# Performance work log

Measured on AMD Instinct MI355X. Metric: run time of the kernel, lower is better.

Reference implementation:

```python
import jax, jax.numpy as jnp
import numpy as np

H = 8          # n_heads
SIZE = 512     # model size
HEAD = SIZE // H
EPS = 1e-5

def _layer_norm(x, g, b):
    mu = jnp.mean(x, axis=-1, keepdims=True)
    var = jnp.var(x, axis=-1, keepdims=True)
    return (x - mu) * jax.lax.rsqrt(var + EPS) * g + b

def setup_inputs() -> dict:
    key = jax.random.key(0)
    ks = jax.random.split(key, 7)
    B, Lq, Lkv, Dq, Dkv = 16, 1024, 1024, 512, 512
    w = 0.02
    return {
        "query": jax.random.normal(ks[0], (B, Lq, Dq), jnp.float32),
        "key_value": jax.random.normal(ks[1], (B, Lkv, Dkv), jnp.float32),
        "Wq": jax.random.normal(ks[2], (SIZE, Dq), jnp.float32) * w,
        "bq": jnp.zeros((SIZE,), jnp.float32),
        "Wk": jax.random.normal(ks[3], (SIZE, Dkv), jnp.float32) * w,
        "bk": jnp.zeros((SIZE,), jnp.float32),
        "Wv": jax.random.normal(ks[4], (SIZE, Dkv), jnp.float32) * w,
        "bv": jnp.zeros((SIZE,), jnp.float32),
        "Wo": jax.random.normal(ks[5], (SIZE, SIZE), jnp.float32) * w,
        "bo": jnp.zeros((SIZE,), jnp.float32),
        "g0": jnp.ones((SIZE,), jnp.float32),
        "b0": jnp.zeros((SIZE,), jnp.float32),
        "g1": jnp.ones((SIZE,), jnp.float32),
        "b1": jnp.zeros((SIZE,), jnp.float32),
    }

def reference(query, key_value, Wq, bq, Wk, bk, Wv, bv, Wo, bo, g0, b0, g1, b1):
    B, Lq, _ = query.shape
    Lkv = key_value.shape[1]
    q = query @ Wq.T + bq            # [B, Lq, SIZE]
    k = key_value @ Wk.T + bk        # [B, Lkv, SIZE]
    v = key_value @ Wv.T + bv        # [B, Lkv, SIZE]
    # split heads along feature dim (equivalent to torch cat(split, 0))
    qh = q.reshape(B, Lq, H, HEAD)
    kh = k.reshape(B, Lkv, H, HEAD)
    vh = v.reshape(B, Lkv, H, HEAD)
    # NOTE: original scales by sqrt(size), NOT sqrt(head_size)
    scores = jnp.einsum('bqhd,bkhd->bhqk', qh, kh) / jnp.sqrt(jnp.float32(SIZE))
    A = jax.nn.softmax(scores, axis=-1)              # [B, H, Lq, Lkv]
    attn = jnp.einsum('bhqk,bkhd->bqhd', A, vh)      # [B, Lq, H, HEAD]
    out = (qh + attn).reshape(B, Lq, SIZE)           # residual uses projected q
    out = _layer_norm(out, g0, b0)
    out = out + jax.nn.relu(out @ Wo.T + bo)
    out = _layer_norm(out, g1, b1)
    return out
```

## Files before the change

### kernel.cpp

```cpp
#include <hip/hip_runtime.h>
#include <hip/hip_bf16.h>


#define HNUM 8
#define MSIZE 512
#define HEADD 64
#define LQ 1024
#define LKV 1024
#define NBATCH 16

typedef unsigned short u16;
typedef __bf16 bf16_t;
typedef bf16_t bf16x8 __attribute__((ext_vector_type(8)));
typedef float f32x4 __attribute__((ext_vector_type(4)));
typedef u16 u16x8 __attribute__((ext_vector_type(8)));

__device__ __forceinline__ u16 f2bf(float f) {
  __bf16 h = (__bf16)f;
  u16 r; __builtin_memcpy(&r, &h, 2); return r;
}

__device__ __forceinline__ bf16x8 ldb8(const void* p) {
  bf16x8 r; __builtin_memcpy(&r, p, 16); return r;
}
__device__ __forceinline__ float4 ldf4(const float* p) {
  float4 v; __builtin_memcpy(&v, p, 16); return v;
}
__device__ __forceinline__ void stf4(float* p, const float4& v) {
  __builtin_memcpy(p, &v, 16);
}

__device__ __forceinline__ void gload16(const u16* g, u16* l) {
  __builtin_amdgcn_global_load_lds((const __attribute__((address_space(1))) void*)g,
                                   (__attribute__((address_space(3))) void*)l,
                                   16, 0, 0);
}


__global__ __launch_bounds__(256) void cvt2_k(const float* __restrict__ a, u16* __restrict__ da,
                                              const float* __restrict__ b, u16* __restrict__ db,
                                              int n) {
  size_t i = ((size_t)blockIdx.x * 256 + threadIdx.x) * 8;
  const float* s; u16* d;
  if (i < (size_t)n) { s = a + i; d = da + i; }
  else               { s = b + (i - n); d = db + (i - n); }
  float4 v0 = ldf4(s), v1 = ldf4(s + 4);
  u16x8 o;
  o[0]=f2bf(v0.x); o[1]=f2bf(v0.y); o[2]=f2bf(v0.z); o[3]=f2bf(v0.w);
  o[4]=f2bf(v1.x); o[5]=f2bf(v1.y); o[6]=f2bf(v1.z); o[7]=f2bf(v1.w);
  __builtin_memcpy(d, &o, 16);
}

__global__ __launch_bounds__(256) void cvt4_k(const float* __restrict__ a0, u16* __restrict__ d0,
                                              const float* __restrict__ a1, u16* __restrict__ d1,
                                              const float* __restrict__ a2, u16* __restrict__ d2,
                                              const float* __restrict__ a3, u16* __restrict__ d3,
                                              int n) {
  size_t i = ((size_t)blockIdx.x * 256 + threadIdx.x) * 8;
  int sel = (int)(i / (size_t)n);
  size_t off = i - (size_t)sel * (size_t)n;
  const float* s = sel == 0 ? a0 : sel == 1 ? a1 : sel == 2 ? a2 : a3;
  u16*         d = sel == 0 ? d0 : sel == 1 ? d1 : sel == 2 ? d2 : d3;
  float4 v0 = ldf4(s + off), v1 = ldf4(s + off + 4);
  u16x8 o;
  o[0]=f2bf(v0.x); o[1]=f2bf(v0.y); o[2]=f2bf(v0.z); o[3]=f2bf(v0.w);
  o[4]=f2bf(v1.x); o[5]=f2bf(v1.y); o[6]=f2bf(v1.z); o[7]=f2bf(v1.w);
  __builtin_memcpy(d + off, &o, 16);
}


template<int MODE>
__global__ __launch_bounds__(256) void gemm_bt_k(
    const u16* __restrict__ A, const u16* __restrict__ W, const float* __restrict__ bias,
    const float* __restrict__ resid, float* __restrict__ outf, u16* __restrict__ outb)
{
  __shared__ u16 As[128 * 32];
  __shared__ u16 Bs[128 * 32];
  const int tid = threadIdx.x;
  const int w = tid >> 6, l = tid & 63;
  const int wr = w >> 1, wc = w & 1;
  const int lo = l & 15, hi = l >> 4;
  const int mb = blockIdx.y, nb = blockIdx.x;

  f32x4 acc[4][4] = {};
  const int s0 = w * 128 + l;

  for (int kt = 0; kt < 16; ++kt) {
    __syncthreads();
#pragma unroll
    for (int c = 0; c < 2; ++c) {
      int s = s0 + c * 64;
      int row = s >> 2, k8 = s & 3;
      const u16* ga = A + (size_t)(mb * 128 + row) * MSIZE + kt * 32 + k8 * 8;
      gload16(ga, &As[(w * 128 + c * 64) * 8]);
      const u16* gw = W + (size_t)(nb * 128 + row) * MSIZE + kt * 32 + k8 * 8;
      gload16(gw, &Bs[(w * 128 + c * 64) * 8]);
    }
    __syncthreads();
    bf16x8 af[4], bfr[4];
#pragma unroll
    for (int i = 0; i < 4; ++i) af[i]  = ldb8(&As[(wr * 64 + i * 16 + lo) * 32 + hi * 8]);
#pragma unroll
    for (int j = 0; j < 4; ++j) bfr[j] = ldb8(&Bs[(wc * 64 + j * 16 + lo) * 32 + hi * 8]);
#pragma unroll
    for (int i = 0; i < 4; ++i)
#pragma unroll
      for (int j = 0; j < 4; ++j)
        acc[i][j] = __builtin_amdgcn_mfma_f32_16x16x32_bf16(af[i], bfr[j], acc[i][j], 0, 0, 0);
  }

  const int nbase = nb * 128 + wc * 64;
  const int mbase = mb * 128 + wr * 64;
  float bj[4];
#pragma unroll
  for (int j = 0; j < 4; ++j) bj[j] = bias[nbase + j * 16 + lo];

  if (MODE == 2) {
    u16* T = As;
#pragma unroll
    for (int j = 0; j < 4; ++j) {
      __syncthreads();
#pragma unroll
      for (int i = 0; i < 4; ++i)
#pragma unroll
        for (int e = 0; e < 4; ++e) {
          int n_local = wc * 16 + lo;
          int m_local = wr * 64 + i * 16 + hi * 4 + e;
          T[n_local * 128 + m_local] = f2bf(acc[i][j][e] + bj[j]);
        }
      __syncthreads();
      int n_local = tid >> 3, m0 = (tid & 7) * 16;
      u16x8 r0, r1;
      __builtin_memcpy(&r0, &T[n_local * 128 + m0], 16);
      __builtin_memcpy(&r1, &T[n_local * 128 + m0 + 8], 16);
      int n_global = nb * 128 + (n_local >> 4) * 64 + j * 16 + (n_local & 15);
      int m_global = mb * 128 + m0;
      int bb = m_global >> 10, tt = m_global & 1023;
      u16* dst = outb + ((size_t)bb * MSIZE + n_global) * LKV + tt;
      __builtin_memcpy(dst, &r0, 16);
      __builtin_memcpy(dst + 8, &r1, 16);
    }
    return;
  }

#pragma unroll
  for (int i = 0; i < 4; ++i) {
#pragma unroll
    for (int j = 0; j < 4; ++j) {
#pragma unroll
      for (int e = 0; e < 4; ++e) {
        int m = mbase + i * 16 + hi * 4 + e;
        int n = nbase + j * 16 + lo;
        float v = acc[i][j][e] + bj[j];
        if (MODE == 0) {
          outf[(size_t)m * MSIZE + n] = v;
          outb[(size_t)m * MSIZE + n] = f2bf(v * 0.04419417382415922f);
        } else if (MODE == 1) {
          outb[(size_t)m * MSIZE + n] = f2bf(v);
        } else {
          float r = resid[(size_t)m * MSIZE + n];
          outf[(size_t)m * MSIZE + n] = r + fmaxf(v, 0.0f);
        }
      }
    }
  }
}


__global__ __launch_bounds__(64) void attn_k(
    const u16* __restrict__ q, const u16* __restrict__ kk, const u16* __restrict__ vt,
    const float* __restrict__ qf, float* __restrict__ out1)
{
  __shared__ u16 P[32 * 68];
  const int l = threadIdx.x;
  const int lo = l & 15, hi = l >> 4;
  const int blk = blockIdx.x;
  const int h = blk & 7, qb = (blk >> 3) & 31, b = blk >> 8;

  const u16* qbase = q  + ((size_t)(b * LQ + qb * 32)) * MSIZE + h * HEADD;
  const u16* kbase = kk + (size_t)b * LKV * MSIZE + h * HEADD;
  const u16* vbase = vt + ((size_t)(b * MSIZE + h * HEADD)) * LKV;

  bf16x8 aq[2][2];
#pragma unroll
  for (int mt = 0; mt < 2; ++mt)
#pragma unroll
    for (int kc = 0; kc < 2; ++kc)
      aq[mt][kc] = ldb8(qbase + (size_t)(mt * 16 + lo) * MSIZE + kc * 32 + hi * 8);

  f32x4 acc[2][4] = {};
  float mrun[2][4], lrun[2][4];
#pragma unroll
  for (int mt = 0; mt < 2; ++mt)
#pragma unroll
    for (int e = 0; e < 4; ++e) { mrun[mt][e] = -1e30f; lrun[mt][e] = 0.0f; }

  for (int n0 = 0; n0 < LKV; n0 += 64) {
    f32x4 S[2][4] = {};
#pragma unroll
    for (int half = 0; half < 2; ++half) {
      bf16x8 bk[2][2];
#pragma unroll
      for (int ntl = 0; ntl < 2; ++ntl)
#pragma unroll
        for (int kc = 0; kc < 2; ++kc)
          bk[ntl][kc] = ldb8(kbase + (size_t)(n0 + (half * 2 + ntl) * 16 + lo) * MSIZE + kc * 32 + hi * 8);
#pragma unroll
      for (int mt = 0; mt < 2; ++mt)
#pragma unroll
        for (int ntl = 0; ntl < 2; ++ntl) {
          int nt = half * 2 + ntl;
          S[mt][nt] = __builtin_amdgcn_mfma_f32_16x16x32_bf16(aq[mt][0], bk[ntl][0], S[mt][nt], 0, 0, 0);
          S[mt][nt] = __builtin_amdgcn_mfma_f32_16x16x32_bf16(aq[mt][1], bk[ntl][1], S[mt][nt], 0, 0, 0);
        }
    }

#pragma unroll
    for (int mt = 0; mt < 2; ++mt) {
#pragma unroll
      for (int e = 0; e < 4; ++e) {
        float cm = fmaxf(fmaxf(S[mt][0][e], S[mt][1][e]), fmaxf(S[mt][2][e], S[mt][3][e]));
#pragma unroll
        for (int msk = 1; msk < 16; msk <<= 1) cm = fmaxf(cm, __shfl_xor(cm, msk));
        float mnew = fmaxf(mrun[mt][e], cm);
        float fs = __expf(mrun[mt][e] - mnew);
        mrun[mt][e] = mnew;
        float p0 = __expf(S[mt][0][e] - mnew);
        float p1 = __expf(S[mt][1][e] - mnew);
        float p2 = __expf(S[mt][2][e] - mnew);
        float p3 = __expf(S[mt][3][e] - mnew);
        float rs = (p0 + p1) + (p2 + p3);
#pragma unroll
        for (int msk = 1; msk < 16; msk <<= 1) rs += __shfl_xor(rs, msk);
        lrun[mt][e] = lrun[mt][e] * fs + rs;
#pragma unroll
        for (int dt = 0; dt < 4; ++dt) acc[mt][dt][e] *= fs;
        int pr = (mt * 16 + hi * 4 + e) * 68 + lo;
        P[pr]      = f2bf(p0);
        P[pr + 16] = f2bf(p1);
        P[pr + 32] = f2bf(p2);
        P[pr + 48] = f2bf(p3);
      }
    }
    __syncthreads();

    bf16x8 pa[2][2];
#pragma unroll
    for (int mt = 0; mt < 2; ++mt)
#pragma unroll
      for (int ks = 0; ks < 2; ++ks)
        pa[mt][ks] = ldb8(&P[(mt * 16 + lo) * 68 + ks * 32 + hi * 8]);
    __syncthreads();

#pragma unroll
    for (int dt = 0; dt < 4; ++dt)
#pragma unroll
      for (int ks = 0; ks < 2; ++ks) {
        bf16x8 bv = ldb8(vbase + (size_t)(dt * 16 + lo) * LKV + n0 + ks * 32 + hi * 8);
#pragma unroll
        for (int mt = 0; mt < 2; ++mt)
          acc[mt][dt] = __builtin_amdgcn_mfma_f32_16x16x32_bf16(pa[mt][ks], bv, acc[mt][dt], 0, 0, 0);
      }
  }

#pragma unroll
  for (int mt = 0; mt < 2; ++mt) {
    float inv[4];
#pragma unroll
    for (int e = 0; e < 4; ++e) inv[e] = 1.0f / lrun[mt][e];
#pragma unroll
    for (int dt = 0; dt < 4; ++dt)
#pragma unroll
      for (int e = 0; e < 4; ++e) {
        size_t m = (size_t)b * LQ + qb * 32 + mt * 16 + hi * 4 + e;
        int n = h * HEADD + dt * 16 + lo;
        float v = acc[mt][dt][e] * inv[e] + qf[m * MSIZE + n];
        out1[m * MSIZE + n] = v;
      }
  }
}


template<int WRITE_BF>
__global__ __launch_bounds__(64) void ln_kk(const float* __restrict__ in, const float* __restrict__ g,
                                            const float* __restrict__ be, float* __restrict__ outf,
                                            u16* __restrict__ outb)
{
  const int row = blockIdx.x, l = threadIdx.x;
  const float* p = in + (size_t)row * MSIZE + l * 8;
  float4 v0 = ldf4(p), v1 = ldf4(p + 4);
  float s  = v0.x + v0.y + v0.z + v0.w + v1.x + v1.y + v1.z + v1.w;
  float s2 = 0.0f;
  s2 = fmaf(v0.x, v0.x, s2); s2 = fmaf(v0.y, v0.y, s2);
  s2 = fmaf(v0.z, v0.z, s2); s2 = fmaf(v0.w, v0.w, s2);
  s2 = fmaf(v1.x, v1.x, s2); s2 = fmaf(v1.y, v1.y, s2);
  s2 = fmaf(v1.z, v1.z, s2); s2 = fmaf(v1.w, v1.w, s2);
#pragma unroll
  for (int m = 1; m < 64; m <<= 1) { s += __shfl_xor(s, m); s2 += __shfl_xor(s2, m); }
  float mu   = s * (1.0f / 512.0f);
  float var  = s2 * (1.0f / 512.0f) - mu * mu;
  float rstd = rsqrtf(var + 1e-5f);

  float4 g0 = ldf4(g + l * 8), g1 = ldf4(g + l * 8 + 4);
  float4 b0 = ldf4(be + l * 8), b1 = ldf4(be + l * 8 + 4);
  float4 o0, o1;
  o0.x = (v0.x - mu) * rstd * g0.x + b0.x;  o0.y = (v0.y - mu) * rstd * g0.y + b0.y;
  o0.z = (v0.z - mu) * rstd * g0.z + b0.z;  o0.w = (v0.w - mu) * rstd * g0.w + b0.w;
  o1.x = (v1.x - mu) * rstd * g1.x + b1.x;  o1.y = (v1.y - mu) * rstd * g1.y + b1.y;
  o1.z = (v1.z - mu) * rstd * g1.z + b1.z;  o1.w = (v1.w - mu) * rstd * g1.w + b1.w;
  float* q = outf + (size_t)row * MSIZE + l * 8;
  stf4(q, o0); stf4(q + 4, o1);
  if (WRITE_BF) {
    u16x8 ob;
    ob[0]=f2bf(o0.x); ob[1]=f2bf(o0.y); ob[2]=f2bf(o0.z); ob[3]=f2bf(o0.w);
    ob[4]=f2bf(o1.x); ob[5]=f2bf(o1.y); ob[6]=f2bf(o1.z); ob[7]=f2bf(o1.w);
    __builtin_memcpy(outb + (size_t)row * MSIZE + l * 8, &ob, 16);
  }
}


extern "C" void kernel_launch(void* const* d_in, const int* in_sizes, int n_in,
                              void* d_out, int out_size, void* d_ws, size_t ws_size,
                              hipStream_t stream) {
  const float* query = (const float*)d_in[0];
  const float* keyv  = (const float*)d_in[1];
  const float* Wq = (const float*)d_in[2];  const float* bq = (const float*)d_in[3];
  const float* Wk = (const float*)d_in[4];  const float* bk = (const float*)d_in[5];
  const float* Wv = (const float*)d_in[6];  const float* bv = (const float*)d_in[7];
  const float* Wo = (const float*)d_in[8];  const float* bo = (const float*)d_in[9];
  const float* g0 = (const float*)d_in[10]; const float* b0 = (const float*)d_in[11];
  const float* g1 = (const float*)d_in[12]; const float* b1 = (const float*)d_in[13];
  float* out = (float*)d_out;

  char* ws = (char*)d_ws;
  const size_t MB = 1u << 20;
  u16*   qbf  = (u16*)(ws + 0);
  u16*   kvbf = (u16*)(ws + 16 * MB);
  u16*   wqb  = (u16*)(ws + 32 * MB);
  u16*   wkb  = wqb + 262144;
  u16*   wvb  = wkb + 262144;
  u16*   wob  = wvb + 262144;
  float* qf32 = (float*)(ws + 36 * MB);
  u16*   qpbf = (u16*)(ws + 68 * MB);
  u16*   kbfp = (u16*)(ws + 84 * MB);
  u16*   vtbf = (u16*)(ws + 100 * MB);
  float* xf32 = (float*)(ws + 0);
  u16*   xbf  = (u16*)(ws + 100 * MB);
  float* yb   = (float*)(ws + 68 * MB);

  const int NTOK = NBATCH * LQ;
  dim3 gg(4, NTOK / 128);

  cvt2_k<<<8192, 256, 0, stream>>>(query, qbf, keyv, kvbf, NTOK * MSIZE);
  cvt4_k<<<512, 256, 0, stream>>>(Wq, wqb, Wk, wkb, Wv, wvb, Wo, wob, MSIZE * MSIZE);
  gemm_bt_k<0><<<gg, 256, 0, stream>>>(qbf,  wqb, bq, nullptr, qf32, qpbf);
  gemm_bt_k<1><<<gg, 256, 0, stream>>>(kvbf, wkb, bk, nullptr, nullptr, kbfp);
  gemm_bt_k<2><<<gg, 256, 0, stream>>>(kvbf, wvb, bv, nullptr, nullptr, vtbf);
  attn_k<<<NBATCH * HNUM * (LQ / 32), 64, 0, stream>>>(qpbf, kbfp, vtbf, qf32, out);
  ln_kk<1><<<NTOK, 64, 0, stream>>>(out, g0, b0, xf32, xbf);
  gemm_bt_k<3><<<gg, 256, 0, stream>>>(xbf, wob, bo, xf32, yb, nullptr);
  ln_kk<0><<<NTOK, 64, 0, stream>>>(yb, g1, b1, out, nullptr);
}
```

Before: 398.0 us.

## Fuse K/V projections, restructure attention with lazy rescale and exp2, batch LN rows

Merges the K and V projection GEMMs into one launch over a doubled N range, with the V half written transposed. The attention kernel now runs four waves per block sharing the K/V head and walks 32-key steps. It folds log2(e) into the Q scale so it can use raw v_exp_f32, and only rescales the running max when any score exceeds it by more than 8, deferring the row-sum reduction to the end. LayerNorm processes four rows per 256-thread block. This cuts launch count and per-step softmax work, at the cost of more loop iterations and a lazy-rescale scheme that must stay numerically safe in bf16.

```diff
diff --git a/kernel.cpp b/kernel.cpp
--- a/kernel.cpp
+++ b/kernel.cpp
@@ -15,11 +15,15 @@
 typedef float f32x4 __attribute__((ext_vector_type(4)));
 typedef u16 u16x8 __attribute__((ext_vector_type(8)));
 
+#define QSCALE 0.06375872338006773f
+
 __device__ __forceinline__ u16 f2bf(float f) {
   __bf16 h = (__bf16)f;
   u16 r; __builtin_memcpy(&r, &h, 2); return r;
 }
-
+__device__ __forceinline__ float fexp2(float x) {
+  float r; asm("v_exp_f32 %0, %1" : "=v"(r) : "v"(x)); return r;
+}
 __device__ __forceinline__ bf16x8 ldb8(const void* p) {
   bf16x8 r; __builtin_memcpy(&r, p, 16); return r;
 }
@@ -29,7 +33,6 @@
 __device__ __forceinline__ void stf4(float* p, const float4& v) {
   __builtin_memcpy(p, &v, 16);
 }
-
 __device__ __forceinline__ void gload16(const u16* g, u16* l) {
   __builtin_amdgcn_global_load_lds((const __attribute__((address_space(1))) void*)g,
                                    (__attribute__((address_space(3))) void*)l,
@@ -72,7 +75,8 @@
 template<int MODE>
 __global__ __launch_bounds__(256) void gemm_bt_k(
     const u16* __restrict__ A, const u16* __restrict__ W, const float* __restrict__ bias,
-    const float* __restrict__ resid, float* __restrict__ outf, u16* __restrict__ outb)
+    const float* __restrict__ bias2, const float* __restrict__ resid,
+    float* __restrict__ outf, u16* __restrict__ outb, u16* __restrict__ outb2)
 {
   __shared__ u16 As[128 * 32];
   __shared__ u16 Bs[128 * 32];
@@ -113,9 +117,12 @@
   const int mbase = mb * 128 + wr * 64;
   float bj[4];
 #pragma unroll
-  for (int j = 0; j < 4; ++j) bj[j] = bias[nbase + j * 16 + lo];
-
-  if (MODE == 2) {
+  for (int j = 0; j < 4; ++j) {
+    int n = nbase + j * 16 + lo;
+    bj[j] = (MODE == 4 && n >= 512) ? bias2[n - 512] : bias[n & 511];
+  }
+
+  if (MODE == 4 && nb >= 4) {
     u16* T = As;
 #pragma unroll
     for (int j = 0; j < 4; ++j) {
@@ -133,10 +140,10 @@
       u16x8 r0, r1;
       __builtin_memcpy(&r0, &T[n_local * 128 + m0], 16);
       __builtin_memcpy(&r1, &T[n_local * 128 + m0 + 8], 16);
-      int n_global = nb * 128 + (n_local >> 4) * 64 + j * 16 + (n_local & 15);
+      int n_global = (nb - 4) * 128 + (n_local >> 4) * 64 + j * 16 + (n_local & 15);
       int m_global = mb * 128 + m0;
       int bb = m_global >> 10, tt = m_global & 1023;
-      u16* dst = outb + ((size_t)bb * MSIZE + n_global) * LKV + tt;
+      u16* dst = outb2 + ((size_t)bb * MSIZE + n_global) * LKV + tt;
       __builtin_memcpy(dst, &r0, 16);
       __builtin_memcpy(dst + 8, &r1, 16);
     }
@@ -154,8 +161,8 @@
         float v = acc[i][j][e] + bj[j];
         if (MODE == 0) {
           outf[(size_t)m * MSIZE + n] = v;
-          outb[(size_t)m * MSIZE + n] = f2bf(v * 0.04419417382415922f);
-        } else if (MODE == 1) {
+          outb[(size_t)m * MSIZE + n] = f2bf(v * QSCALE);
+        } else if (MODE == 4) {
           outb[(size_t)m * MSIZE + n] = f2bf(v);
         } else {
           float r = resid[(size_t)m * MSIZE + n];
@@ -167,15 +174,18 @@
 }
 
 
-__global__ __launch_bounds__(64) void attn_k(
+__global__ __launch_bounds__(256, 4) void attn_k(
     const u16* __restrict__ q, const u16* __restrict__ kk, const u16* __restrict__ vt,
     const float* __restrict__ qf, float* __restrict__ out1)
 {
-  __shared__ u16 P[32 * 68];
-  const int l = threadIdx.x;
+  __shared__ u16 P[4][1296];
+  const int tid = threadIdx.x;
+  const int w = tid >> 6, l = tid & 63;
   const int lo = l & 15, hi = l >> 4;
   const int blk = blockIdx.x;
-  const int h = blk & 7, qb = (blk >> 3) & 31, b = blk >> 8;
+  const int h = blk & 7, qg = (blk >> 3) & 7, b = blk >> 6;
+  const int qb = qg * 4 + w;
+  u16* Pw = P[w];
 
   const u16* qbase = q  + ((size_t)(b * LQ + qb * 32)) * MSIZE + h * HEADD;
   const u16* kbase = kk + (size_t)b * LKV * MSIZE + h * HEADD;
@@ -189,85 +199,101 @@
       aq[mt][kc] = ldb8(qbase + (size_t)(mt * 16 + lo) * MSIZE + kc * 32 + hi * 8);
 
   f32x4 acc[2][4] = {};
-  float mrun[2][4], lrun[2][4];
+  float ps[2][4] = {};
+  float mrun[2][4] = {};
+
+  for (int n0 = 0; n0 < LKV; n0 += 32) {
+    bf16x8 bk[2][2];
+#pragma unroll
+    for (int ntl = 0; ntl < 2; ++ntl)
+#pragma unroll
+      for (int kc = 0; kc < 2; ++kc)
+        bk[ntl][kc] = ldb8(kbase + (size_t)(n0 + 2 * lo + ntl) * MSIZE + kc * 32 + hi * 8);
+
+    f32x4 S[2][2] = {};
+#pragma unroll
+    for (int mt = 0; mt < 2; ++mt)
+#pragma unroll
+      for (int ntl = 0; ntl < 2; ++ntl) {
+        S[mt][ntl] = __builtin_amdgcn_mfma_f32_16x16x32_bf16(aq[mt][0], bk[ntl][0], S[mt][ntl], 0, 0, 0);
+        S[mt][ntl] = __builtin_amdgcn_mfma_f32_16x16x32_bf16(aq[mt][1], bk[ntl][1], S[mt][ntl], 0, 0, 0);
+      }
+
+    int ok = 1;
+    float cmr[2][4];
+#pragma unroll
+    for (int mt = 0; mt < 2; ++mt)
+#pragma unroll
+      for (int e = 0; e < 4; ++e) {
+        cmr[mt][e] = fmaxf(S[mt][0][e], S[mt][1][e]);
+        ok &= (cmr[mt][e] <= mrun[mt][e] + 8.0f);
+      }
+
+    if (__all(ok)) {
+#pragma unroll
+      for (int mt = 0; mt < 2; ++mt)
+#pragma unroll
+        for (int e = 0; e < 4; ++e) {
+          float m0 = mrun[mt][e];
+          float p0 = fexp2(S[mt][0][e] - m0);
+          float p1 = fexp2(S[mt][1][e] - m0);
+          ps[mt][e] += p0 + p1;
+          unsigned wv = (unsigned)f2bf(p0) | ((unsigned)f2bf(p1) << 16);
+          *reinterpret_cast<unsigned*>(Pw + (mt * 16 + hi * 4 + e) * 40 + 2 * lo) = wv;
+        }
+    } else {
+#pragma unroll
+      for (int mt = 0; mt < 2; ++mt)
+#pragma unroll
+        for (int e = 0; e < 4; ++e) {
+          float cm = cmr[mt][e];
+#pragma unroll
+          for (int msk = 1; msk < 16; msk <<= 1) cm = fmaxf(cm, __shfl_xor(cm, msk));
+          float mnew = fmaxf(mrun[mt][e], cm);
+          float fs = fexp2(mrun[mt][e] - mnew);
+          mrun[mt][e] = mnew;
+          ps[mt][e] *= fs;
+#pragma unroll
+          for (int dt = 0; dt < 4; ++dt) acc[mt][dt][e] *= fs;
+          float p0 = fexp2(S[mt][0][e] - mnew);
+          float p1 = fexp2(S[mt][1][e] - mnew);
+          ps[mt][e] += p0 + p1;
+          unsigned wv = (unsigned)f2bf(p0) | ((unsigned)f2bf(p1) << 16);
+          *reinterpret_cast<unsigned*>(Pw + (mt * 16 + hi * 4 + e) * 40 + 2 * lo) = wv;
+        }
+    }
+
+    __syncthreads();
+    bf16x8 pa[2];
+#pragma unroll
+    for (int mt = 0; mt < 2; ++mt) pa[mt] = ldb8(&Pw[(mt * 16 + lo) * 40 + hi * 8]);
+    __syncthreads();
+
+#pragma unroll
+    for (int dt = 0; dt < 4; ++dt) {
+      bf16x8 bv = ldb8(vbase + (size_t)(dt * 16 + lo) * LKV + n0 + hi * 8);
+#pragma unroll
+      for (int mt = 0; mt < 2; ++mt)
+        acc[mt][dt] = __builtin_amdgcn_mfma_f32_16x16x32_bf16(pa[mt], bv, acc[mt][dt], 0, 0, 0);
+    }
+  }
+
+  float lr[2][4];
 #pragma unroll
   for (int mt = 0; mt < 2; ++mt)
 #pragma unroll
-    for (int e = 0; e < 4; ++e) { mrun[mt][e] = -1e30f; lrun[mt][e] = 0.0f; }
-
-  for (int n0 = 0; n0 < LKV; n0 += 64) {
-    f32x4 S[2][4] = {};
-#pragma unroll
-    for (int half = 0; half < 2; ++half) {
-      bf16x8 bk[2][2];
-#pragma unroll
-      for (int ntl = 0; ntl < 2; ++ntl)
-#pragma unroll
-        for (int kc = 0; kc < 2; ++kc)
-          bk[ntl][kc] = ldb8(kbase + (size_t)(n0 + (half * 2 + ntl) * 16 + lo) * MSIZE + kc * 32 + hi * 8);
-#pragma unroll
-      for (int mt = 0; mt < 2; ++mt)
-#pragma unroll
-        for (int ntl = 0; ntl < 2; ++ntl) {
-          int nt = half * 2 + ntl;
-          S[mt][nt] = __builtin_amdgcn_mfma_f32_16x16x32_bf16(aq[mt][0], bk[ntl][0], S[mt][nt], 0, 0, 0);
-          S[mt][nt] = __builtin_amdgcn_mfma_f32_16x16x32_bf16(aq[mt][1], bk[ntl][1], S[mt][nt], 0, 0, 0);
-        }
-    }
-
-#pragma unroll
-    for (int mt = 0; mt < 2; ++mt) {
-#pragma unroll
-      for (int e = 0; e < 4; ++e) {
-        float cm = fmaxf(fmaxf(S[mt][0][e], S[mt][1][e]), fmaxf(S[mt][2][e], S[mt][3][e]));
-#pragma unroll
-        for (int msk = 1; msk < 16; msk <<= 1) cm = fmaxf(cm, __shfl_xor(cm, msk));
-        float mnew = fmaxf(mrun[mt][e], cm);
-        float fs = __expf(mrun[mt][e] - mnew);
-        mrun[mt][e] = mnew;
-        float p0 = __expf(S[mt][0][e] - mnew);
-        float p1 = __expf(S[mt][1][e] - mnew);
-        float p2 = __expf(S[mt][2][e] - mnew);
-        float p3 = __expf(S[mt][3][e] - mnew);
-        float rs = (p0 + p1) + (p2 + p3);
-#pragma unroll
-        for (int msk = 1; msk < 16; msk <<= 1) rs += __shfl_xor(rs, msk);
-        lrun[mt][e] = lrun[mt][e] * fs + rs;
-#pragma unroll
-        for (int dt = 0; dt < 4; ++dt) acc[mt][dt][e] *= fs;
-        int pr = (mt * 16 + hi * 4 + e) * 68 + lo;
-        P[pr]      = f2bf(p0);
-        P[pr + 16] = f2bf(p1);
-        P[pr + 32] = f2bf(p2);
-        P[pr + 48] = f2bf(p3);
-      }
-    }
-    __syncthreads();
-
-    bf16x8 pa[2][2];
-#pragma unroll
-    for (int mt = 0; mt < 2; ++mt)
-#pragma unroll
-      for (int ks = 0; ks < 2; ++ks)
-        pa[mt][ks] = ldb8(&P[(mt * 16 + lo) * 68 + ks * 32 + hi * 8]);
-    __syncthreads();
-
-#pragma unroll
-    for (int dt = 0; dt < 4; ++dt)
-#pragma unroll
-      for (int ks = 0; ks < 2; ++ks) {
-        bf16x8 bv = ldb8(vbase + (size_t)(dt * 16 + lo) * LKV + n0 + ks * 32 + hi * 8);
-#pragma unroll
-        for (int mt = 0; mt < 2; ++mt)
-          acc[mt][dt] = __builtin_amdgcn_mfma_f32_16x16x32_bf16(pa[mt][ks], bv, acc[mt][dt], 0, 0, 0);
-      }
-  }
+    for (int e = 0; e < 4; ++e) {
+      float s = ps[mt][e];
+#pragma unroll
+      for (int msk = 1; msk < 16; msk <<= 1) s += __shfl_xor(s, msk);
+      lr[mt][e] = s;
+    }
 
 #pragma unroll
   for (int mt = 0; mt < 2; ++mt) {
     float inv[4];
 #pragma unroll
-    for (int e = 0; e < 4; ++e) inv[e] = 1.0f / lrun[mt][e];
+    for (int e = 0; e < 4; ++e) inv[e] = 1.0f / lr[mt][e];
 #pragma unroll
     for (int dt = 0; dt < 4; ++dt)
 #pragma unroll
@@ -282,11 +308,12 @@
 
 
 template<int WRITE_BF>
-__global__ __launch_bounds__(64) void ln_kk(const float* __restrict__ in, const float* __restrict__ g,
-                                            const float* __restrict__ be, float* __restrict__ outf,
-                                            u16* __restrict__ outb)
+__global__ __launch_bounds__(256) void ln_kk(const float* __restrict__ in, const float* __restrict__ g,
+                                             const float* __restrict__ be, float* __restrict__ outf,
+                                             u16* __restrict__ outb)
 {
-  const int row = blockIdx.x, l = threadIdx.x;
+  const int row = blockIdx.x * 4 + (threadIdx.x >> 6);
+  const int l = threadIdx.x & 63;
   const float* p = in + (size_t)row * MSIZE + l * 8;
   float4 v0 = ldf4(p), v1 = ldf4(p + 4);
   float s  = v0.x + v0.y + v0.z + v0.w + v1.x + v1.y + v1.z + v1.w;
@@ -350,14 +377,14 @@
 
   const int NTOK = NBATCH * LQ;
   dim3 gg(4, NTOK / 128);
+  dim3 gkv(8, NTOK / 128);
 
   cvt2_k<<<8192, 256, 0, stream>>>(query, qbf, keyv, kvbf, NTOK * MSIZE);
   cvt4_k<<<512, 256, 0, stream>>>(Wq, wqb, Wk, wkb, Wv, wvb, Wo, wob, MSIZE * MSIZE);
-  gemm_bt_k<0><<<gg, 256, 0, stream>>>(qbf,  wqb, bq, nullptr, qf32, qpbf);
-  gemm_bt_k<1><<<gg, 256, 0, stream>>>(kvbf, wkb, bk, nullptr, nullptr, kbfp);
-  gemm_bt_k<2><<<gg, 256, 0, stream>>>(kvbf, wvb, bv, nullptr, nullptr, vtbf);
-  attn_k<<<NBATCH * HNUM * (LQ / 32), 64, 0, stream>>>(qpbf, kbfp, vtbf, qf32, out);
-  ln_kk<1><<<NTOK, 64, 0, stream>>>(out, g0, b0, xf32, xbf);
-  gemm_bt_k<3><<<gg, 256, 0, stream>>>(xbf, wob, bo, xf32, yb, nullptr);
-  ln_kk<0><<<NTOK, 64, 0, stream>>>(yb, g1, b1, out, nullptr);
-}
+  gemm_bt_k<0><<<gg, 256, 0, stream>>>(qbf, wqb, bq, nullptr, nullptr, qf32, qpbf, nullptr);
+  gemm_bt_k<4><<<gkv, 256, 0, stream>>>(kvbf, wkb, bk, bv, nullptr, nullptr, kbfp, vtbf);
+  attn_k<<<NBATCH * HNUM * (LQ / 32) / 4, 256, 0, stream>>>(qpbf, kbfp, vtbf, qf32, out);
+  ln_kk<1><<<NTOK / 4, 256, 0, stream>>>(out, g0, b0, xf32, xbf);
+  gemm_bt_k<3><<<gg, 256, 0, stream>>>(xbf, wob, bo, nullptr, xf32, yb, nullptr, nullptr);
+  ln_kk<0><<<NTOK / 4, 256, 0, stream>>>(yb, g1, b1, out, nullptr);
+}
```

Result: slower. 428.3 us (+7.6%).
